# Kernel tuning notes

Measured on AMD Instinct MI355X. Metric: run time of the kernel, lower is better.

## Reference

```python
import jax, jax.numpy as jnp
import numpy as np
from jax import lax

B, T, D, H = 32, 512, 768, 768


def setup_inputs() -> dict:
    key = jax.random.key(0)
    ks = jax.random.split(key, 8)
    s_in = 1.0 / np.sqrt(D)
    s_h = 1.0 / np.sqrt(H)
    return {
        "x": jax.random.normal(ks[0], (B, T, D), jnp.float32),
        "Wx0": jax.random.normal(ks[1], (D, 4 * H), jnp.float32) * s_in,
        "Wh0": jax.random.normal(ks[2], (H, 4 * H), jnp.float32) * s_h,
        "b0": jnp.zeros((4 * H,), jnp.float32),
        "Wx1": jax.random.normal(ks[3], (H, 4 * H), jnp.float32) * s_h,
        "Wh1": jax.random.normal(ks[4], (H, 4 * H), jnp.float32) * s_h,
        "b1": jnp.zeros((4 * H,), jnp.float32),
        "ln_scale": jnp.ones((H,), jnp.float32),
        "ln_bias": jnp.zeros((H,), jnp.float32),
    }


def _lstm_layer(x, Wx, Wh, b):
    # x: [B, T, Din]; flax LSTMCell gate order (i, f, g, o); input proj has no bias.
    bsz = x.shape[0]
    hdim = Wh.shape[0]
    xg = jnp.einsum("btd,dg->btg", x, Wx)  # precompute input projections [B,T,4H]

    def step(carry, xg_t):
        c, h = carry
        gates = xg_t + h @ Wh + b  # [B, 4H]
        i, f, g, o = jnp.split(gates, 4, axis=-1)
        i = jax.nn.sigmoid(i)
        f = jax.nn.sigmoid(f)
        g = jnp.tanh(g)
        o = jax.nn.sigmoid(o)
        c = f * c + i * g
        h = o * jnp.tanh(c)
        return (c, h), h

    init = (jnp.zeros((bsz, hdim), x.dtype), jnp.zeros((bsz, hdim), x.dtype))
    _, hs = lax.scan(step, init, jnp.swapaxes(xg, 0, 1))  # hs: [T, B, H]
    return jnp.swapaxes(hs, 0, 1)


def _layer_norm(x, scale, bias, eps=1e-6):
    mean = jnp.mean(x, axis=-1, keepdims=True)
    var = jnp.mean(jnp.square(x - mean), axis=-1, keepdims=True)
    return (x - mean) * lax.rsqrt(var + eps) * scale + bias


def reference(x, Wx0, Wh0, b0, Wx1, Wh1, b1, ln_scale, ln_bias):
    # Dropout is identity (deterministic=True, eval mode).
    h = _lstm_layer(x, Wx0, Wh0, b0)
    h = _lstm_layer(h, Wx1, Wh1, b1)
    return _layer_norm(h, ln_scale, ln_bias)
```

## Files before the change

### kernel.cpp

```cpp
#include <hip/hip_runtime.h>
#include <stdint.h>
#include <cstdio>

typedef unsigned short u16;
typedef __attribute__((ext_vector_type(8))) __bf16 bf16x8;
typedef __attribute__((ext_vector_type(4))) float f32x4;
typedef __attribute__((ext_vector_type(4))) int i32x4;

#define AGENT __HIP_MEMORY_SCOPE_AGENT

__device__ __forceinline__ float bf2f(u16 u) {
  unsigned int x = ((unsigned int)u) << 16;
  return __builtin_bit_cast(float, x);
}
__device__ __forceinline__ u16 f2bf(float f) {
  unsigned int x = __builtin_bit_cast(unsigned int, f);
  unsigned int r = (x + 0x7fffu + ((x >> 16) & 1u)) >> 16;
  return (u16)r;
}
__device__ __forceinline__ float sigm(float x) { return 1.f / (1.f + __expf(-x)); }
__device__ __forceinline__ float tanh_f(float x) { return 1.f - 2.f / (__expf(2.f * x) + 1.f); }

__global__ __launch_bounds__(256) void k_cvt(const float* __restrict__ in, u16* __restrict__ out, int n4) {
  int i = blockIdx.x * 256 + threadIdx.x;
  if (i >= n4) return;
  float4 f = ((const float4*)in)[i];
  ushort4 o;
  o.x = f2bf(f.x); o.y = f2bf(f.y); o.z = f2bf(f.z); o.w = f2bf(f.w);
  ((ushort4*)out)[i] = o;
}

__global__ __launch_bounds__(256) void k_pack_wx(const float* __restrict__ Wx, u16* __restrict__ Bp) {
  int idx = blockIdx.x * 256 + threadIdx.x;
  if (idx >= 2359296) return;
  int j = idx & 7;
  int l = (idx >> 3) & 63;
  int t = idx >> 9;
  int kt = t % 24, nt = t / 24;
  int k = kt * 32 + (l >> 4) * 8 + j;
  int n = nt * 16 + (l & 15);
  Bp[idx] = f2bf(Wx[(size_t)k * 3072 + n]);
}

__global__ __launch_bounds__(256) void k_pack_wh(const float* __restrict__ Wh, u16* __restrict__ Wp) {
  int idx = blockIdx.x * 256 + threadIdx.x;
  if (idx >= 2359296) return;
  int j = idx & 7;
  int l = (idx >> 3) & 63;
  int t = idx >> 9;
  int kt = t % 24;
  int tmp = t / 24;
  int nt = tmp % 6, w = tmp / 6;
  int k = kt * 32 + (l >> 4) * 8 + j;
  int cc = l & 15;
  int vi = cc >> 2, q = cc & 3;
  int gcol = q * 768 + w * 24 + nt * 4 + vi;
  Wp[idx] = f2bf(Wh[(size_t)k * 3072 + gcol]);
}

__global__ __launch_bounds__(256, 2) void k_gemm(const u16* __restrict__ A, const u16* __restrict__ Bp,
                                                 u16* __restrict__ C) {
  const int bid = blockIdx.x;
  const int bm = bid & 127, bn = bid >> 7;
  const int tid = threadIdx.x, lane = tid & 63, wv = tid >> 6;
  const int wm = wv >> 1, wn = wv & 1;
  const int row0 = bm * 128 + wm * 64;
  const int col0 = bn * 128 + wn * 64;
  const int rlo = lane & 15, rhi = lane >> 4;
  f32x4 acc[4][4] = {};
  const u16* Ab = A + (size_t)(row0 + rlo) * 768 + rhi * 8;
  const u16* Bb = Bp + ((size_t)(bn * 8 + wn * 4) * 24 * 64 + lane) * 8;
#pragma unroll 2
  for (int kt = 0; kt < 24; ++kt) {
    bf16x8 a[4], b[4];
#pragma unroll
    for (int i = 0; i < 4; ++i) a[i] = *(const bf16x8*)(Ab + (size_t)i * 16 * 768 + kt * 32);
#pragma unroll
    for (int j = 0; j < 4; ++j) b[j] = *(const bf16x8*)(Bb + (size_t)j * 24 * 64 * 8 + (size_t)kt * 64 * 8);
#pragma unroll
    for (int i = 0; i < 4; ++i)
#pragma unroll
      for (int j = 0; j < 4; ++j)
        acc[i][j] = __builtin_amdgcn_mfma_f32_16x16x32_bf16(a[i], b[j], acc[i][j], 0, 0, 0);
  }
#pragma unroll
  for (int i = 0; i < 4; ++i)
#pragma unroll
    for (int j = 0; j < 4; ++j)
#pragma unroll
      for (int r = 0; r < 4; ++r) {
        int row = row0 + i * 16 + rhi * 4 + r;
        int col = col0 + j * 16 + rlo;
        C[(size_t)row * 3072 + col] = f2bf(acc[i][j][r]);
      }
}

__global__ __launch_bounds__(384) void k_rec(
    const u16* __restrict__ xg,
    const u16* __restrict__ Whp,
    const float* __restrict__ bias,
    int* hbuf,
    u16* __restrict__ hout_bf,
    float* __restrict__ hout_f,
    int layer) {
  __shared__ __align__(16) int hlds[4 * 400];

  const int wid = blockIdx.x, g = wid & 7, w = wid >> 3;
  const int tid = threadIdx.x, lane = tid & 63, wv = tid >> 6;

  bf16x8 bregE[12], bregO[12];
  {
    const u16* bp = Whp + (((size_t)(w * 6 + wv) * 24) * 64 + lane) * 8;
#pragma unroll
    for (int kk = 0; kk < 12; ++kk) {
      bregE[kk] = *(const bf16x8*)(bp + (size_t)(2 * kk) * 512);
      bregO[kk] = *(const bf16x8*)(bp + (size_t)(2 * kk + 1) * 512);
    }
  }

  const bool cellt = (lane & 15) < 4;
  const int vi = lane >> 4, r = lane & 3;
  const int unit = w * 24 + wv * 4 + vi;
  const int seq = g * 4 + r;
  float bv0 = 0, bv1 = 0, bv2 = 0, bv3 = 0, xv0 = 0, xv1 = 0, xv2 = 0, xv3 = 0;
  if (cellt) {
    bv0 = bias[unit]; bv1 = bias[768 + unit]; bv2 = bias[1536 + unit]; bv3 = bias[2304 + unit];
    const u16* xr = xg + (size_t)seq * 512 * 3072;
    xv0 = bf2f(xr[unit]); xv1 = bf2f(xr[768 + unit]);
    xv2 = bf2f(xr[1536 + unit]); xv3 = bf2f(xr[2304 + unit]);
  }
  float cst = 0.f;
  const int sl = (lane & 15) < 4 ? (lane & 15) : 3;
  const int abase = sl * 400 + (lane >> 4) * 4;
  const int c = tid;
  const int hrow = c / 96, hcol = (c % 96) * 4;
  int guard = 0;

  __syncthreads();

  for (int t = 0; t < 512; ++t) {
    const int expect = t;
    int* src = hbuf + (size_t)(g * 2 + (t & 1)) * 3072;
    const int* p0 = src + 8 * c;
    const int* p1 = src + 8 * c + 4;
    i32x4 v0, v1;
    for (;;) {
      asm volatile("global_load_dwordx4 %0, %2, off sc0 sc1\n\t"
                   "global_load_dwordx4 %1, %3, off sc0 sc1\n\t"
                   "s_waitcnt vmcnt(0)"
                   : "=&v"(v0), "=&v"(v1)
                   : "v"(p0), "v"(p1)
                   : "memory");
      bool ok = true;
#pragma unroll
      for (int j = 0; j < 4; ++j)
        ok = ok && ((v0[j] & 0xffff) == expect) && ((v1[j] & 0xffff) == expect);
      if (ok || ++guard > (1 << 22)) break;
    }
    __syncthreads();

    {
      int4 pk;
      pk.x = (int)(((unsigned)v0[0] >> 16) | ((unsigned)v0[1] & 0xffff0000u));
      pk.y = (int)(((unsigned)v0[2] >> 16) | ((unsigned)v0[3] & 0xffff0000u));
      pk.z = (int)(((unsigned)v1[0] >> 16) | ((unsigned)v1[1] & 0xffff0000u));
      pk.w = (int)(((unsigned)v1[2] >> 16) | ((unsigned)v1[3] & 0xffff0000u));
      *(int4*)&hlds[hrow * 400 + hcol] = pk;
    }
    __syncthreads();

    f32x4 a0 = {0, 0, 0, 0}, a1 = {0, 0, 0, 0};
#pragma unroll
    for (int kk = 0; kk < 12; ++kk) {
      bf16x8 afe = *(const bf16x8*)(hlds + abase + (2 * kk) * 16);
      bf16x8 afo = *(const bf16x8*)(hlds + abase + (2 * kk + 1) * 16);
      a0 = __builtin_amdgcn_mfma_f32_16x16x32_bf16(bregE[kk], afe, a0, 0, 0, 0);
      a1 = __builtin_amdgcn_mfma_f32_16x16x32_bf16(bregO[kk], afo, a1, 0, 0, 0);
    }
    a0 += a1;

    if (cellt) {
      float p0g = xv0 + a0[0] + bv0;
      float p1g = xv1 + a0[1] + bv1;
      float p2g = xv2 + a0[2] + bv2;
      float p3g = xv3 + a0[3] + bv3;
      float ig = sigm(p0g), fg = sigm(p1g), gg = tanh_f(p2g), og = sigm(p3g);
      cst = fg * cst + ig * gg;
      float h = og * tanh_f(cst);
      int* dst = hbuf + (size_t)(g * 2 + ((t + 1) & 1)) * 3072 + r * 768 + unit;
      int val = (int)(((unsigned)f2bf(h) << 16) | (unsigned)(t + 1));
      __hip_atomic_store(dst, val, __ATOMIC_RELAXED, AGENT);
      size_t o = ((size_t)seq * 512 + t) * 768 + unit;
      if (layer == 0) hout_bf[o] = f2bf(h); else hout_f[o] = h;
      if (t + 1 < 512) {
        const u16* xr = xg + ((size_t)seq * 512 + t + 1) * 3072;
        xv0 = bf2f(xr[unit]); xv1 = bf2f(xr[768 + unit]);
        xv2 = bf2f(xr[1536 + unit]); xv3 = bf2f(xr[2304 + unit]);
      }
    }
  }
}

__global__ __launch_bounds__(256) void k_ln(const float* __restrict__ in, const float* __restrict__ sc,
                                            const float* __restrict__ bi, float* __restrict__ out) {
  const int row = blockIdx.x, tid = threadIdx.x;
  const float* x = in + (size_t)row * 768;
  float v0 = x[tid], v1 = x[tid + 256], v2 = x[tid + 512];
  float s = v0 + v1 + v2;
  float s2 = v0 * v0 + v1 * v1 + v2 * v2;
#pragma unroll
  for (int off = 32; off >= 1; off >>= 1) {
    s += __shfl_xor(s, off);
    s2 += __shfl_xor(s2, off);
  }
  __shared__ float red[8];
  const int wv = tid >> 6;
  if ((tid & 63) == 0) { red[wv] = s; red[4 + wv] = s2; }
  __syncthreads();
  s = red[0] + red[1] + red[2] + red[3];
  s2 = red[4] + red[5] + red[6] + red[7];
  float mean = s * (1.f / 768.f);
  float var = s2 * (1.f / 768.f) - mean * mean;
  float rs = rsqrtf(var + 1e-6f);
  float* o = out + (size_t)row * 768;
  o[tid] = (v0 - mean) * rs * sc[tid] + bi[tid];
  o[tid + 256] = (v1 - mean) * rs * sc[tid + 256] + bi[tid + 256];
  o[tid + 512] = (v2 - mean) * rs * sc[tid + 512] + bi[tid + 512];
}

extern "C" void kernel_launch(void* const* d_in, const int* in_sizes, int n_in,
                              void* d_out, int out_size, void* d_ws, size_t ws_size,
                              hipStream_t stream) {
  const float* x   = (const float*)d_in[0];
  const float* Wx0 = (const float*)d_in[1];
  const float* Wh0 = (const float*)d_in[2];
  const float* b0  = (const float*)d_in[3];
  const float* Wx1 = (const float*)d_in[4];
  const float* Wh1 = (const float*)d_in[5];
  const float* b1  = (const float*)d_in[6];
  const float* lns = (const float*)d_in[7];
  const float* lnb = (const float*)d_in[8];
  float* out = (float*)d_out;

  char* p = (char*)d_ws;
  auto alloc = [&](size_t bytes) {
    char* r = p;
    p += (bytes + 255) & ~(size_t)255;
    return r;
  };
  u16* xg    = (u16*)alloc(16384ull * 3072 * 2);
  u16* xbf   = (u16*)alloc(16384ull * 768 * 2);
  u16* h0bf  = (u16*)alloc(16384ull * 768 * 2);
  u16* Wxp0  = (u16*)alloc(2359296ull * 2);
  u16* Wxp1  = (u16*)alloc(2359296ull * 2);
  u16* Whp0  = (u16*)alloc(2359296ull * 2);
  u16* Whp1  = (u16*)alloc(2359296ull * 2);
  char* sync0 = alloc(196608ull * 2);
  int* hbuf0 = (int*)sync0;
  int* hbuf1 = (int*)(sync0 + 196608);

  if ((size_t)(p - (char*)d_ws) > ws_size) {
    fprintf(stderr, "kernel_launch: ws too small: need %zu have %zu\n",
            (size_t)(p - (char*)d_ws), ws_size);
    return;
  }

  hipMemsetAsync(sync0, 0, 196608ull * 2, stream);
  k_cvt<<<12288, 256, 0, stream>>>(x, xbf, 3145728);
  k_pack_wx<<<9216, 256, 0, stream>>>(Wx0, Wxp0);
  k_pack_wx<<<9216, 256, 0, stream>>>(Wx1, Wxp1);
  k_pack_wh<<<9216, 256, 0, stream>>>(Wh0, Whp0);
  k_pack_wh<<<9216, 256, 0, stream>>>(Wh1, Whp1);

  k_gemm<<<3072, 256, 0, stream>>>(xbf, Wxp0, xg);
  k_rec<<<256, 384, 0, stream>>>(xg, Whp0, b0, hbuf0, h0bf, nullptr, 0);
  k_gemm<<<3072, 256, 0, stream>>>(h0bf, Wxp1, xg);
  k_rec<<<256, 384, 0, stream>>>(xg, Whp1, b1, hbuf1, nullptr, (float*)d_out, 1);
  k_ln<<<16384, 256, 0, stream>>>((const float*)d_out, lns, lnb, out);
}
```

Baseline: 2.141 ms.

## Halve recurrent grid by giving each wave two hidden-unit tiles

The persistent LSTM recurrence kernel now runs on 128 blocks instead of 256. Each wave holds two 16-column weight tiles in registers and computes two hidden units per cell thread. The Wh packing is remapped to match. This halves the number of blocks that poll and synchronise on the cross-block h buffer each timestep, at the cost of twice the register footprint for resident weights and twice the MFMA and gate work per wave on the serial critical path.

```diff
diff --git a/kernel.cpp b/kernel.cpp
--- a/kernel.cpp
+++ b/kernel.cpp
@@ -50,12 +50,12 @@
   int t = idx >> 9;
   int kt = t % 24;
   int tmp = t / 24;
-  int nt = tmp % 6, w = tmp / 6;
+  int nt = tmp % 12, w = tmp / 12;
   int k = kt * 32 + (l >> 4) * 8 + j;
   int cc = l & 15;
   int vi = cc >> 2, q = cc & 3;
-  int gcol = q * 768 + w * 24 + nt * 4 + vi;
-  Wp[idx] = f2bf(Wh[(size_t)k * 3072 + gcol]);
+  int unit = w * 48 + (nt >> 1) * 8 + (nt & 1) * 4 + vi;
+  Wp[idx] = f2bf(Wh[(size_t)k * 3072 + q * 768 + unit]);
 }
 
 __global__ __launch_bounds__(256, 2) void k_gemm(const u16* __restrict__ A, const u16* __restrict__ Bp,
@@ -108,28 +108,36 @@
   const int wid = blockIdx.x, g = wid & 7, w = wid >> 3;
   const int tid = threadIdx.x, lane = tid & 63, wv = tid >> 6;
 
-  bf16x8 bregE[12], bregO[12];
+  bf16x8 wE0[12], wO0[12], wE1[12], wO1[12];
   {
-    const u16* bp = Whp + (((size_t)(w * 6 + wv) * 24) * 64 + lane) * 8;
+    const u16* bp0 = Whp + (((size_t)(w * 12 + wv * 2) * 24) * 64 + lane) * 8;
+    const u16* bp1 = bp0 + (size_t)24 * 512;
 #pragma unroll
     for (int kk = 0; kk < 12; ++kk) {
-      bregE[kk] = *(const bf16x8*)(bp + (size_t)(2 * kk) * 512);
-      bregO[kk] = *(const bf16x8*)(bp + (size_t)(2 * kk + 1) * 512);
+      wE0[kk] = *(const bf16x8*)(bp0 + (size_t)(2 * kk) * 512);
+      wO0[kk] = *(const bf16x8*)(bp0 + (size_t)(2 * kk + 1) * 512);
+      wE1[kk] = *(const bf16x8*)(bp1 + (size_t)(2 * kk) * 512);
+      wO1[kk] = *(const bf16x8*)(bp1 + (size_t)(2 * kk + 1) * 512);
     }
   }
 
   const bool cellt = (lane & 15) < 4;
   const int vi = lane >> 4, r = lane & 3;
-  const int unit = w * 24 + wv * 4 + vi;
+  const int unit0 = w * 48 + wv * 8 + vi;
+  const int unit1 = unit0 + 4;
   const int seq = g * 4 + r;
-  float bv0 = 0, bv1 = 0, bv2 = 0, bv3 = 0, xv0 = 0, xv1 = 0, xv2 = 0, xv3 = 0;
+  float bA0 = 0, bA1 = 0, bA2 = 0, bA3 = 0, bB0 = 0, bB1 = 0, bB2 = 0, bB3 = 0;
+  float xA0 = 0, xA1 = 0, xA2 = 0, xA3 = 0, xB0 = 0, xB1 = 0, xB2 = 0, xB3 = 0;
   if (cellt) {
-    bv0 = bias[unit]; bv1 = bias[768 + unit]; bv2 = bias[1536 + unit]; bv3 = bias[2304 + unit];
+    bA0 = bias[unit0]; bA1 = bias[768 + unit0]; bA2 = bias[1536 + unit0]; bA3 = bias[2304 + unit0];
+    bB0 = bias[unit1]; bB1 = bias[768 + unit1]; bB2 = bias[1536 + unit1]; bB3 = bias[2304 + unit1];
     const u16* xr = xg + (size_t)seq * 512 * 3072;
-    xv0 = bf2f(xr[unit]); xv1 = bf2f(xr[768 + unit]);
-    xv2 = bf2f(xr[1536 + unit]); xv3 = bf2f(xr[2304 + unit]);
-  }
-  float cst = 0.f;
+    xA0 = bf2f(xr[unit0]); xA1 = bf2f(xr[768 + unit0]);
+    xA2 = bf2f(xr[1536 + unit0]); xA3 = bf2f(xr[2304 + unit0]);
+    xB0 = bf2f(xr[unit1]); xB1 = bf2f(xr[768 + unit1]);
+    xB2 = bf2f(xr[1536 + unit1]); xB3 = bf2f(xr[2304 + unit1]);
+  }
+  float cst0 = 0.f, cst1 = 0.f;
   const int sl = (lane & 15) < 4 ? (lane & 15) : 3;
   const int abase = sl * 400 + (lane >> 4) * 4;
   const int c = tid;
@@ -169,33 +177,53 @@
     }
     __syncthreads();
 
-    f32x4 a0 = {0, 0, 0, 0}, a1 = {0, 0, 0, 0};
+    f32x4 a0 = {0, 0, 0, 0}, a1 = {0, 0, 0, 0}, a2 = {0, 0, 0, 0}, a3 = {0, 0, 0, 0};
 #pragma unroll
     for (int kk = 0; kk < 12; ++kk) {
       bf16x8 afe = *(const bf16x8*)(hlds + abase + (2 * kk) * 16);
       bf16x8 afo = *(const bf16x8*)(hlds + abase + (2 * kk + 1) * 16);
-      a0 = __builtin_amdgcn_mfma_f32_16x16x32_bf16(bregE[kk], afe, a0, 0, 0, 0);
-      a1 = __builtin_amdgcn_mfma_f32_16x16x32_bf16(bregO[kk], afo, a1, 0, 0, 0);
+      a0 = __builtin_amdgcn_mfma_f32_16x16x32_bf16(wE0[kk], afe, a0, 0, 0, 0);
+      a1 = __builtin_amdgcn_mfma_f32_16x16x32_bf16(wO0[kk], afo, a1, 0, 0, 0);
+      a2 = __builtin_amdgcn_mfma_f32_16x16x32_bf16(wE1[kk], afe, a2, 0, 0, 0);
+      a3 = __builtin_amdgcn_mfma_f32_16x16x32_bf16(wO1[kk], afo, a3, 0, 0, 0);
     }
     a0 += a1;
+    a2 += a3;
 
     if (cellt) {
-      float p0g = xv0 + a0[0] + bv0;
-      float p1g = xv1 + a0[1] + bv1;
-      float p2g = xv2 + a0[2] + bv2;
-      float p3g = xv3 + a0[3] + bv3;
+      float p0g = xA0 + a0[0] + bA0;
+      float p1g = xA1 + a0[1] + bA1;
+      float p2g = xA2 + a0[2] + bA2;
+      float p3g = xA3 + a0[3] + bA3;
       float ig = sigm(p0g), fg = sigm(p1g), gg = tanh_f(p2g), og = sigm(p3g);
-      cst = fg * cst + ig * gg;
-      float h = og * tanh_f(cst);
-      int* dst = hbuf + (size_t)(g * 2 + ((t + 1) & 1)) * 3072 + r * 768 + unit;
-      int val = (int)(((unsigned)f2bf(h) << 16) | (unsigned)(t + 1));
-      __hip_atomic_store(dst, val, __ATOMIC_RELAXED, AGENT);
-      size_t o = ((size_t)seq * 512 + t) * 768 + unit;
-      if (layer == 0) hout_bf[o] = f2bf(h); else hout_f[o] = h;
+      cst0 = fg * cst0 + ig * gg;
+      float h0 = og * tanh_f(cst0);
+      p0g = xB0 + a2[0] + bB0;
+      p1g = xB1 + a2[1] + bB1;
+      p2g = xB2 + a2[2] + bB2;
+      p3g = xB3 + a2[3] + bB3;
+      ig = sigm(p0g); fg = sigm(p1g); gg = tanh_f(p2g); og = sigm(p3g);
+      cst1 = fg * cst1 + ig * gg;
+      float h1 = og * tanh_f(cst1);
+      int* dstb = hbuf + (size_t)(g * 2 + ((t + 1) & 1)) * 3072 + r * 768;
+      int val0 = (int)(((unsigned)f2bf(h0) << 16) | (unsigned)(t + 1));
+      int val1 = (int)(((unsigned)f2bf(h1) << 16) | (unsigned)(t + 1));
+      __hip_atomic_store(dstb + unit0, val0, __ATOMIC_RELAXED, AGENT);
+      __hip_atomic_store(dstb + unit1, val1, __ATOMIC_RELAXED, AGENT);
+      size_t ob = ((size_t)seq * 512 + t) * 768;
+      if (layer == 0) {
+        hout_bf[ob + unit0] = f2bf(h0);
+        hout_bf[ob + unit1] = f2bf(h1);
+      } else {
+        hout_f[ob + unit0] = h0;
+        hout_f[ob + unit1] = h1;
+      }
       if (t + 1 < 512) {
         const u16* xr = xg + ((size_t)seq * 512 + t + 1) * 3072;
-        xv0 = bf2f(xr[unit]); xv1 = bf2f(xr[768 + unit]);
-        xv2 = bf2f(xr[1536 + unit]); xv3 = bf2f(xr[2304 + unit]);
+        xA0 = bf2f(xr[unit0]); xA1 = bf2f(xr[768 + unit0]);
+        xA2 = bf2f(xr[1536 + unit0]); xA3 = bf2f(xr[2304 + unit0]);
+        xB0 = bf2f(xr[unit1]); xB1 = bf2f(xr[768 + unit1]);
+        xB2 = bf2f(xr[1536 + unit1]); xB3 = bf2f(xr[2304 + unit1]);
       }
     }
   }
@@ -273,8 +301,8 @@
   k_pack_wh<<<9216, 256, 0, stream>>>(Wh1, Whp1);
 
   k_gemm<<<3072, 256, 0, stream>>>(xbf, Wxp0, xg);
-  k_rec<<<256, 384, 0, stream>>>(xg, Whp0, b0, hbuf0, h0bf, nullptr, 0);
+  k_rec<<<128, 384, 0, stream>>>(xg, Whp0, b0, hbuf0, h0bf, nullptr, 0);
   k_gemm<<<3072, 256, 0, stream>>>(h0bf, Wxp1, xg);
-  k_rec<<<256, 384, 0, stream>>>(xg, Whp1, b1, hbuf1, nullptr, (float*)d_out, 1);
+  k_rec<<<128, 384, 0, stream>>>(xg, Whp1, b1, hbuf1, nullptr, (float*)d_out, 1);
   k_ln<<<16384, 256, 0, stream>>>((const float*)d_out, lns, lnb, out);
 }
```

Measured after the change: 4.593 ms. +114.5%, slower.

## Fuse both LSTM layers into one wavefront-pipelined persistent recurrence kernel

Applied to the files above, without the earlier changes.

Replaces the two sequential recurrent kernels and the layer-1 input GEMM with a single persistent kernel. At each step it advances layer 0 at time t and layer 1 at time t-1, so the two layers form a diagonal wavefront. Layer 1's input projection is computed on the fly from h0 using Wx1 tiles held in LDS (about 144KB per block), and the layer-0 bf16 hidden-state buffer is no longer written. This removes one full recurrence's serial latency and the intermediate GEMM. In exchange each step does more MFMA work and more register and LDS traffic, and it must poll two sync buffers, which may lengthen the per-step critical path.

```diff
diff --git a/kernel.cpp b/kernel.cpp
--- a/kernel.cpp
+++ b/kernel.cpp
@@ -95,26 +95,39 @@
       }
 }
 
-__global__ __launch_bounds__(384) void k_rec(
+__global__ __launch_bounds__(384) void k_rec2(
     const u16* __restrict__ xg,
-    const u16* __restrict__ Whp,
-    const float* __restrict__ bias,
-    int* hbuf,
-    u16* __restrict__ hout_bf,
-    float* __restrict__ hout_f,
-    int layer) {
-  __shared__ __align__(16) int hlds[4 * 400];
+    const u16* __restrict__ Whp0,
+    const u16* __restrict__ Whp1,
+    const u16* __restrict__ Wxp1,
+    const float* __restrict__ b0,
+    const float* __restrict__ b1,
+    int* hbuf0,
+    int* hbuf1,
+    float* __restrict__ out) {
+  __shared__ __align__(16) u16 wxlds[73728];
+  __shared__ __align__(16) int h0lds[1600];
+  __shared__ __align__(16) int h1lds[1600];
 
   const int wid = blockIdx.x, g = wid & 7, w = wid >> 3;
   const int tid = threadIdx.x, lane = tid & 63, wv = tid >> 6;
 
-  bf16x8 bregE[12], bregO[12];
   {
-    const u16* bp = Whp + (((size_t)(w * 6 + wv) * 24) * 64 + lane) * 8;
+    const int4* s4 = (const int4*)(Wxp1 + (size_t)w * 73728);
+    int4* d4 = (int4*)wxlds;
+    for (int i = tid; i < 9216; i += 384) d4[i] = s4[i];
+  }
+
+  bf16x8 w0E[12], w0O[12], w1E[12], w1O[12];
+  {
+    const u16* bp0 = Whp0 + (((size_t)(w * 6 + wv) * 24) * 64 + lane) * 8;
+    const u16* bp1 = Whp1 + (((size_t)(w * 6 + wv) * 24) * 64 + lane) * 8;
 #pragma unroll
     for (int kk = 0; kk < 12; ++kk) {
-      bregE[kk] = *(const bf16x8*)(bp + (size_t)(2 * kk) * 512);
-      bregO[kk] = *(const bf16x8*)(bp + (size_t)(2 * kk + 1) * 512);
+      w0E[kk] = *(const bf16x8*)(bp0 + (size_t)(2 * kk) * 512);
+      w0O[kk] = *(const bf16x8*)(bp0 + (size_t)(2 * kk + 1) * 512);
+      w1E[kk] = *(const bf16x8*)(bp1 + (size_t)(2 * kk) * 512);
+      w1O[kk] = *(const bf16x8*)(bp1 + (size_t)(2 * kk + 1) * 512);
     }
   }
 
@@ -122,80 +135,147 @@
   const int vi = lane >> 4, r = lane & 3;
   const int unit = w * 24 + wv * 4 + vi;
   const int seq = g * 4 + r;
-  float bv0 = 0, bv1 = 0, bv2 = 0, bv3 = 0, xv0 = 0, xv1 = 0, xv2 = 0, xv3 = 0;
+  float bA0 = 0, bA1 = 0, bA2 = 0, bA3 = 0;
+  float bB0 = 0, bB1 = 0, bB2 = 0, bB3 = 0;
+  float xv0 = 0, xv1 = 0, xv2 = 0, xv3 = 0;
   if (cellt) {
-    bv0 = bias[unit]; bv1 = bias[768 + unit]; bv2 = bias[1536 + unit]; bv3 = bias[2304 + unit];
+    bA0 = b0[unit]; bA1 = b0[768 + unit]; bA2 = b0[1536 + unit]; bA3 = b0[2304 + unit];
+    bB0 = b1[unit]; bB1 = b1[768 + unit]; bB2 = b1[1536 + unit]; bB3 = b1[2304 + unit];
     const u16* xr = xg + (size_t)seq * 512 * 3072;
     xv0 = bf2f(xr[unit]); xv1 = bf2f(xr[768 + unit]);
     xv2 = bf2f(xr[1536 + unit]); xv3 = bf2f(xr[2304 + unit]);
   }
-  float cst = 0.f;
+  float cst0 = 0.f, cst1 = 0.f;
   const int sl = (lane & 15) < 4 ? (lane & 15) : 3;
   const int abase = sl * 400 + (lane >> 4) * 4;
   const int c = tid;
   const int hrow = c / 96, hcol = (c % 96) * 4;
+  const u16* wx_base = wxlds + ((size_t)wv * 24 * 64 + lane) * 8;
   int guard = 0;
 
   __syncthreads();
 
-  for (int t = 0; t < 512; ++t) {
-    const int expect = t;
-    int* src = hbuf + (size_t)(g * 2 + (t & 1)) * 3072;
-    const int* p0 = src + 8 * c;
-    const int* p1 = src + 8 * c + 4;
-    i32x4 v0, v1;
-    for (;;) {
-      asm volatile("global_load_dwordx4 %0, %2, off sc0 sc1\n\t"
-                   "global_load_dwordx4 %1, %3, off sc0 sc1\n\t"
-                   "s_waitcnt vmcnt(0)"
-                   : "=&v"(v0), "=&v"(v1)
-                   : "v"(p0), "v"(p1)
-                   : "memory");
-      bool ok = true;
-#pragma unroll
-      for (int j = 0; j < 4; ++j)
-        ok = ok && ((v0[j] & 0xffff) == expect) && ((v1[j] & 0xffff) == expect);
-      if (ok || ++guard > (1 << 22)) break;
+  for (int t = 0; t <= 512; ++t) {
+    const int e0 = t, e1 = t - 1;
+    int* s0 = hbuf0 + (size_t)(g * 2 + (t & 1)) * 3072;
+    int* s1 = hbuf1 + (size_t)(g * 2 + ((t - 1) & 1)) * 3072;
+    const int* p00 = s0 + 8 * c;
+    const int* p01 = p00 + 4;
+    const int* p10 = s1 + 8 * c;
+    const int* p11 = p10 + 4;
+    i32x4 va, vb, vc, vd;
+    if (t >= 1) {
+      for (;;) {
+        asm volatile("global_load_dwordx4 %0, %4, off sc0 sc1\n\t"
+                     "global_load_dwordx4 %1, %5, off sc0 sc1\n\t"
+                     "global_load_dwordx4 %2, %6, off sc0 sc1\n\t"
+                     "global_load_dwordx4 %3, %7, off sc0 sc1\n\t"
+                     "s_waitcnt vmcnt(0)"
+                     : "=&v"(va), "=&v"(vb), "=&v"(vc), "=&v"(vd)
+                     : "v"(p00), "v"(p01), "v"(p10), "v"(p11)
+                     : "memory");
+        bool ok = true;
+#pragma unroll
+        for (int j = 0; j < 4; ++j)
+          ok = ok && ((va[j] & 0xffff) == e0) && ((vb[j] & 0xffff) == e0) &&
+               ((vc[j] & 0xffff) == e1) && ((vd[j] & 0xffff) == e1);
+        if (ok || ++guard > (1 << 22)) break;
+      }
+    } else {
+      for (;;) {
+        asm volatile("global_load_dwordx4 %0, %2, off sc0 sc1\n\t"
+                     "global_load_dwordx4 %1, %3, off sc0 sc1\n\t"
+                     "s_waitcnt vmcnt(0)"
+                     : "=&v"(va), "=&v"(vb)
+                     : "v"(p00), "v"(p01)
+                     : "memory");
+        bool ok = true;
+#pragma unroll
+        for (int j = 0; j < 4; ++j)
+          ok = ok && ((va[j] & 0xffff) == e0) && ((vb[j] & 0xffff) == e0);
+        if (ok || ++guard > (1 << 22)) break;
+      }
     }
     __syncthreads();
 
     {
       int4 pk;
-      pk.x = (int)(((unsigned)v0[0] >> 16) | ((unsigned)v0[1] & 0xffff0000u));
-      pk.y = (int)(((unsigned)v0[2] >> 16) | ((unsigned)v0[3] & 0xffff0000u));
-      pk.z = (int)(((unsigned)v1[0] >> 16) | ((unsigned)v1[1] & 0xffff0000u));
-      pk.w = (int)(((unsigned)v1[2] >> 16) | ((unsigned)v1[3] & 0xffff0000u));
-      *(int4*)&hlds[hrow * 400 + hcol] = pk;
+      pk.x = (int)(((unsigned)va[0] >> 16) | ((unsigned)va[1] & 0xffff0000u));
+      pk.y = (int)(((unsigned)va[2] >> 16) | ((unsigned)va[3] & 0xffff0000u));
+      pk.z = (int)(((unsigned)vb[0] >> 16) | ((unsigned)vb[1] & 0xffff0000u));
+      pk.w = (int)(((unsigned)vb[2] >> 16) | ((unsigned)vb[3] & 0xffff0000u));
+      *(int4*)&h0lds[hrow * 400 + hcol] = pk;
+      if (t >= 1) {
+        pk.x = (int)(((unsigned)vc[0] >> 16) | ((unsigned)vc[1] & 0xffff0000u));
+        pk.y = (int)(((unsigned)vc[2] >> 16) | ((unsigned)vc[3] & 0xffff0000u));
+        pk.z = (int)(((unsigned)vd[0] >> 16) | ((unsigned)vd[1] & 0xffff0000u));
+        pk.w = (int)(((unsigned)vd[2] >> 16) | ((unsigned)vd[3] & 0xffff0000u));
+        *(int4*)&h1lds[hrow * 400 + hcol] = pk;
+      }
     }
     __syncthreads();
 
-    f32x4 a0 = {0, 0, 0, 0}, a1 = {0, 0, 0, 0};
-#pragma unroll
-    for (int kk = 0; kk < 12; ++kk) {
-      bf16x8 afe = *(const bf16x8*)(hlds + abase + (2 * kk) * 16);
-      bf16x8 afo = *(const bf16x8*)(hlds + abase + (2 * kk + 1) * 16);
-      a0 = __builtin_amdgcn_mfma_f32_16x16x32_bf16(bregE[kk], afe, a0, 0, 0, 0);
-      a1 = __builtin_amdgcn_mfma_f32_16x16x32_bf16(bregO[kk], afo, a1, 0, 0, 0);
-    }
-    a0 += a1;
-
-    if (cellt) {
-      float p0g = xv0 + a0[0] + bv0;
-      float p1g = xv1 + a0[1] + bv1;
-      float p2g = xv2 + a0[2] + bv2;
-      float p3g = xv3 + a0[3] + bv3;
-      float ig = sigm(p0g), fg = sigm(p1g), gg = tanh_f(p2g), og = sigm(p3g);
-      cst = fg * cst + ig * gg;
-      float h = og * tanh_f(cst);
-      int* dst = hbuf + (size_t)(g * 2 + ((t + 1) & 1)) * 3072 + r * 768 + unit;
-      int val = (int)(((unsigned)f2bf(h) << 16) | (unsigned)(t + 1));
-      __hip_atomic_store(dst, val, __ATOMIC_RELAXED, AGENT);
-      size_t o = ((size_t)seq * 512 + t) * 768 + unit;
-      if (layer == 0) hout_bf[o] = f2bf(h); else hout_f[o] = h;
-      if (t + 1 < 512) {
-        const u16* xr = xg + ((size_t)seq * 512 + t + 1) * 3072;
-        xv0 = bf2f(xr[unit]); xv1 = bf2f(xr[768 + unit]);
-        xv2 = bf2f(xr[1536 + unit]); xv3 = bf2f(xr[2304 + unit]);
+    if (t < 512) {
+      f32x4 a0 = {0, 0, 0, 0}, a1 = {0, 0, 0, 0};
+#pragma unroll
+      for (int kk = 0; kk < 12; ++kk) {
+        bf16x8 he = *(const bf16x8*)(h0lds + abase + (2 * kk) * 16);
+        bf16x8 ho = *(const bf16x8*)(h0lds + abase + (2 * kk + 1) * 16);
+        a0 = __builtin_amdgcn_mfma_f32_16x16x32_bf16(w0E[kk], he, a0, 0, 0, 0);
+        a1 = __builtin_amdgcn_mfma_f32_16x16x32_bf16(w0O[kk], ho, a1, 0, 0, 0);
+      }
+      a0 += a1;
+      if (cellt) {
+        float p0g = xv0 + a0[0] + bA0;
+        float p1g = xv1 + a0[1] + bA1;
+        float p2g = xv2 + a0[2] + bA2;
+        float p3g = xv3 + a0[3] + bA3;
+        float ig = sigm(p0g), fg = sigm(p1g), gg = tanh_f(p2g), og = sigm(p3g);
+        cst0 = fg * cst0 + ig * gg;
+        float h = og * tanh_f(cst0);
+        int* dst = hbuf0 + (size_t)(g * 2 + ((t + 1) & 1)) * 3072 + r * 768 + unit;
+        int val = (int)(((unsigned)f2bf(h) << 16) | (unsigned)(t + 1));
+        __hip_atomic_store(dst, val, __ATOMIC_RELAXED, AGENT);
+        if (t + 1 < 512) {
+          const u16* xr = xg + ((size_t)seq * 512 + t + 1) * 3072;
+          xv0 = bf2f(xr[unit]); xv1 = bf2f(xr[768 + unit]);
+          xv2 = bf2f(xr[1536 + unit]); xv3 = bf2f(xr[2304 + unit]);
+        }
+      }
+    }
+    __builtin_amdgcn_sched_barrier(0);
+
+    if (t >= 1) {
+      f32x4 c0 = {0, 0, 0, 0}, c1 = {0, 0, 0, 0};
+#pragma unroll
+      for (int kk = 0; kk < 12; ++kk) {
+        bf16x8 xe = *(const bf16x8*)(wx_base + (size_t)(2 * kk) * 512);
+        bf16x8 xo = *(const bf16x8*)(wx_base + (size_t)(2 * kk + 1) * 512);
+        bf16x8 he = *(const bf16x8*)(h0lds + abase + (2 * kk) * 16);
+        bf16x8 ho = *(const bf16x8*)(h0lds + abase + (2 * kk + 1) * 16);
+        c0 = __builtin_amdgcn_mfma_f32_16x16x32_bf16(xe, he, c0, 0, 0, 0);
+        c1 = __builtin_amdgcn_mfma_f32_16x16x32_bf16(xo, ho, c1, 0, 0, 0);
+      }
+#pragma unroll
+      for (int kk = 0; kk < 12; ++kk) {
+        bf16x8 he = *(const bf16x8*)(h1lds + abase + (2 * kk) * 16);
+        bf16x8 ho = *(const bf16x8*)(h1lds + abase + (2 * kk + 1) * 16);
+        c0 = __builtin_amdgcn_mfma_f32_16x16x32_bf16(w1E[kk], he, c0, 0, 0, 0);
+        c1 = __builtin_amdgcn_mfma_f32_16x16x32_bf16(w1O[kk], ho, c1, 0, 0, 0);
+      }
+      c0 += c1;
+      if (cellt) {
+        float p0g = c0[0] + bB0;
+        float p1g = c0[1] + bB1;
+        float p2g = c0[2] + bB2;
+        float p3g = c0[3] + bB3;
+        float ig = sigm(p0g), fg = sigm(p1g), gg = tanh_f(p2g), og = sigm(p3g);
+        cst1 = fg * cst1 + ig * gg;
+        float h = og * tanh_f(cst1);
+        int* dst = hbuf1 + (size_t)(g * 2 + (t & 1)) * 3072 + r * 768 + unit;
+        int val = (int)(((unsigned)f2bf(h) << 16) | (unsigned)t);
+        __hip_atomic_store(dst, val, __ATOMIC_RELAXED, AGENT);
+        out[((size_t)seq * 512 + (t - 1)) * 768 + unit] = h;
       }
     }
   }
@@ -250,11 +330,10 @@
   };
   u16* xg    = (u16*)alloc(16384ull * 3072 * 2);
   u16* xbf   = (u16*)alloc(16384ull * 768 * 2);
-  u16* h0bf  = (u16*)alloc(16384ull * 768 * 2);
   u16* Wxp0  = (u16*)alloc(2359296ull * 2);
-  u16* Wxp1  = (u16*)alloc(2359296ull * 2);
-  u16* Whp0  = (u16*)alloc(2359296ull * 2);
-  u16* Whp1  = (u16*)alloc(2359296ull * 2);
+  u16* Whp0s = (u16*)alloc(2359296ull * 2);
+  u16* Whp1s = (u16*)alloc(2359296ull * 2);
+  u16* Wxp1s = (u16*)alloc(2359296ull * 2);
   char* sync0 = alloc(196608ull * 2);
   int* hbuf0 = (int*)sync0;
   int* hbuf1 = (int*)(sync0 + 196608);
@@ -268,13 +347,11 @@
   hipMemsetAsync(sync0, 0, 196608ull * 2, stream);
   k_cvt<<<12288, 256, 0, stream>>>(x, xbf, 3145728);
   k_pack_wx<<<9216, 256, 0, stream>>>(Wx0, Wxp0);
-  k_pack_wx<<<9216, 256, 0, stream>>>(Wx1, Wxp1);
-  k_pack_wh<<<9216, 256, 0, stream>>>(Wh0, Whp0);
-  k_pack_wh<<<9216, 256, 0, stream>>>(Wh1, Whp1);
+  k_pack_wh<<<9216, 256, 0, stream>>>(Wh0, Whp0s);
+  k_pack_wh<<<9216, 256, 0, stream>>>(Wh1, Whp1s);
+  k_pack_wh<<<9216, 256, 0, stream>>>(Wx1, Wxp1s);
 
   k_gemm<<<3072, 256, 0, stream>>>(xbf, Wxp0, xg);
-  k_rec<<<256, 384, 0, stream>>>(xg, Whp0, b0, hbuf0, h0bf, nullptr, 0);
-  k_gemm<<<3072, 256, 0, stream>>>(h0bf, Wxp1, xg);
-  k_rec<<<256, 384, 0, stream>>>(xg, Whp1, b1, hbuf1, nullptr, (float*)d_out, 1);
+  k_rec2<<<256, 384, 0, stream>>>(xg, Whp0s, Whp1s, Wxp1s, b0, b1, hbuf0, hbuf1, (float*)d_out);
   k_ln<<<16384, 256, 0, stream>>>((const float*)d_out, lns, lnb, out);
 }
```

New measurement: 4.432 ms. 2.07x slower.
